# Optimization experiments

Hardware: AMD Instinct MI355X
Metric: run time of the kernel (lower is better)

The kernel has to match this reference:

```python
import jax, jax.numpy as jnp
import numpy as np

N = 50000
E = 640000
F_IN = 96
H1 = 128
H2 = 128
NUM_CLASSES = 256
NGRAM = 3
D1 = 32
L2_EPS = 1e-12


def _prop(xt, src, dst, ew):
    # weighted scatter-add aggregation: out[dst] += ew * xt[src]
    return jax.ops.segment_sum(ew[:, None] * xt[src], dst, num_segments=N)


def _digcn_layer(x, W_mi, W_mo, W_sk, b_mi, b_mo, b_si, b_so, C_in, C_out,
                 ei_in, ew_in, ei_out, ew_out):
    x_sk = x @ W_sk  # skip transform shared by in/out branches
    ic = (_prop(x @ W_mi, ei_in[0], ei_in[1], ew_in) + b_mi
          + _prop(x_sk, ei_in[0], ei_in[1], ew_in) + b_si)
    oc = (_prop(x @ W_mo, ei_out[0], ei_out[1], ew_out) + b_mo
          + _prop(x_sk, ei_out[0], ei_out[1], ew_out) + b_so)
    return C_in * ic + C_out * oc  # C_* are [N,1] vector coefficients


def setup_inputs() -> dict:
    key = jax.random.key(0)
    ks = jax.random.split(key, 32)
    s = 0.05
    d = {
        'x': jax.random.normal(ks[0], (N, F_IN), dtype=jnp.float32),
        'edge_index_in': jax.random.randint(ks[1], (2, E), 0, N, dtype=jnp.int32),
        'edge_weight_in': jax.random.uniform(ks[2], (E,), dtype=jnp.float32),
        'edge_index_out': jax.random.randint(ks[3], (2, E), 0, N, dtype=jnp.int32),
        'edge_weight_out': jax.random.uniform(ks[4], (E,), dtype=jnp.float32),
        'pe_table': jax.random.normal(ks[5], (NGRAM, D1), dtype=jnp.float32) * s,
    }
    dims = [(F_IN, H1), (H1, H1), (H1, H2)]
    ki = 6
    for li, (di, do) in enumerate(dims, start=1):
        d[f'W{li}_main_in'] = jax.random.normal(ks[ki], (di, do), dtype=jnp.float32) * s; ki += 1
        d[f'W{li}_main_out'] = jax.random.normal(ks[ki], (di, do), dtype=jnp.float32) * s; ki += 1
        d[f'W{li}_skip'] = jax.random.normal(ks[ki], (di, do), dtype=jnp.float32) * s; ki += 1
        d[f'b{li}_main_in'] = jax.random.normal(ks[ki], (do,), dtype=jnp.float32) * s; ki += 1
        d[f'b{li}_main_out'] = jax.random.normal(ks[ki], (do,), dtype=jnp.float32) * s; ki += 1
        d[f'b{li}_skip_in'] = jax.random.normal(ks[ki], (do,), dtype=jnp.float32) * s; ki += 1
        d[f'b{li}_skip_out'] = jax.random.normal(ks[ki], (do,), dtype=jnp.float32) * s; ki += 1
        d[f'C{li}_in'] = 1.0 + jax.random.normal(ks[ki], (N, 1), dtype=jnp.float32) * 0.02; ki += 1
        d[f'C{li}_out'] = 1.0 + jax.random.normal(ks[ki], (N, 1), dtype=jnp.float32) * 0.02; ki += 1
    k2 = jax.random.split(ks[ki], 4)
    d['res1_W'] = jax.random.normal(k2[0], (F_IN, H1), dtype=jnp.float32) * s
    d['res1_b'] = jax.random.normal(k2[1], (H1,), dtype=jnp.float32) * s
    d['dec_W'] = jax.random.normal(k2[2], (H2, NUM_CLASSES), dtype=jnp.float32) * s
    d['dec_b'] = jax.random.normal(k2[3], (NUM_CLASSES,), dtype=jnp.float32) * s
    return d


def reference(x, edge_index_in, edge_weight_in, edge_index_out, edge_weight_out, pe_table,
              W1_main_in, W1_main_out, W1_skip, b1_main_in, b1_main_out, b1_skip_in, b1_skip_out, C1_in, C1_out,
              W2_main_in, W2_main_out, W2_skip, b2_main_in, b2_main_out, b2_skip_in, b2_skip_out, C2_in, C2_out,
              W3_main_in, W3_main_out, W3_skip, b3_main_in, b3_main_out, b3_skip_in, b3_skip_out, C3_in, C3_out,
              res1_W, res1_b, dec_W, dec_b):
    # learnable positional encoding: x viewed as [N, ngram, d1] + pe[pos]
    x = (x.reshape(-1, NGRAM, D1) + pe_table[None]).reshape(-1, NGRAM * D1)

    h1 = _digcn_layer(x, W1_main_in, W1_main_out, W1_skip, b1_main_in, b1_main_out,
                      b1_skip_in, b1_skip_out, C1_in, C1_out,
                      edge_index_in, edge_weight_in, edge_index_out, edge_weight_out)
    h1 = jax.nn.relu(h1 + (x @ res1_W + res1_b))  # residual_proj_1 (96 -> 128)

    h2 = _digcn_layer(h1, W2_main_in, W2_main_out, W2_skip, b2_main_in, b2_main_out,
                      b2_skip_in, b2_skip_out, C2_in, C2_out,
                      edge_index_in, edge_weight_in, edge_index_out, edge_weight_out)
    h2 = jax.nn.relu(h2 + h1)  # identity residual (128 == 128)

    h3 = _digcn_layer(h2, W3_main_in, W3_main_out, W3_skip, b3_main_in, b3_main_out,
                      b3_skip_in, b3_skip_out, C3_in, C3_out,
                      edge_index_in, edge_weight_in, edge_index_out, edge_weight_out)
    h3 = h3 + h2  # residual_proj_3 is Identity (hidden1 == hidden2)

    norm = jnp.maximum(jnp.linalg.norm(h3, axis=1, keepdims=True), L2_EPS)
    emb = h3 / norm  # F.normalize, eps=1e-12
    logits = emb @ dec_W + dec_b
    return jax.nn.log_softmax(logits, axis=-1), emb
```

## Files before the change

kernel.cpp:

```cpp
#include <hip/hip_runtime.h>
#include <hip/hip_bf16.h>

typedef unsigned short ushort_t;
typedef __attribute__((ext_vector_type(8))) short bf16x8;
typedef __attribute__((ext_vector_type(4))) float f32x4;

__device__ __forceinline__ float bf2f(ushort_t u) {
    union { unsigned int i; float f; } v; v.i = ((unsigned int)u) << 16; return v.f;
}
__device__ __forceinline__ ushort_t f2bf(float f) {
    unsigned int u = __float_as_uint(f);
    unsigned int r = u + 0x7FFFu + ((u >> 16) & 1u);
    return (ushort_t)(r >> 16);
}
__device__ __forceinline__ float ldf(const void* p, size_t i, int isf) {
    return isf ? ((const float*)p)[i] : bf2f(((const ushort_t*)p)[i]);
}

__global__ void probe_dtype_k(const void* __restrict__ x, int* __restrict__ flag) {
    int t = threadIdx.x;
    const float* xf = (const float*)x;
    int bad = 0;
    for (int i = t; i < 2048; i += 256) {
        unsigned int u = __float_as_uint(xf[i]);
        unsigned int e = (u >> 23) & 0xFFu;
        if (e >= 0xC0u) bad = 1;
    }
    __shared__ int s_bad;
    if (t == 0) s_bad = 0;
    __syncthreads();
    if (bad) atomicOr(&s_bad, 1);
    __syncthreads();
    if (t == 0) flag[0] = s_bad ? 0 : 1;
}

__global__ void count_dst_k(const int* __restrict__ ei, int* __restrict__ cnt, int E) {
    int e = blockIdx.x * 256 + threadIdx.x;
    if (e < E) atomicAdd(&cnt[ei[E + e]], 1);
}

__global__ __launch_bounds__(256) void scan1_k(const int* __restrict__ cntA, const int* __restrict__ cntB,
                                               int* __restrict__ offA, int* __restrict__ offB,
                                               int* __restrict__ sums, int n, int nChunks) {
    int set = blockIdx.y;
    const int* cnt = set ? cntB : cntA;
    int* off = set ? offB : offA;
    __shared__ int s[256];
    int t = threadIdx.x;
    int idx = blockIdx.x * 1024 + t * 4;
    int v[4];
#pragma unroll
    for (int i = 0; i < 4; ++i) v[i] = (idx + i < n) ? cnt[idx + i] : 0;
    int tsum = v[0] + v[1] + v[2] + v[3];
    s[t] = tsum;
    __syncthreads();
    for (int d = 1; d < 256; d <<= 1) {
        int x = (t >= d) ? s[t - d] : 0;
        __syncthreads();
        s[t] += x;
        __syncthreads();
    }
    int run = s[t] - tsum;
    if (t == 255) sums[set * nChunks + blockIdx.x] = s[255];
#pragma unroll
    for (int i = 0; i < 4; ++i) { if (idx + i < n) off[idx + i] = run; run += v[i]; }
}

__global__ __launch_bounds__(256) void scan2_k(int* __restrict__ sums, int nChunks) {
    __shared__ int s[256];
    int t = threadIdx.x;
    for (int set = 0; set < 2; ++set) {
        int v = (t < nChunks) ? sums[set * nChunks + t] : 0;
        s[t] = v;
        __syncthreads();
        for (int d = 1; d < 256; d <<= 1) {
            int x = (t >= d) ? s[t - d] : 0;
            __syncthreads();
            s[t] += x;
            __syncthreads();
        }
        if (t < nChunks) sums[set * nChunks + t] = s[t] - v;
        __syncthreads();
    }
}

__global__ __launch_bounds__(256) void scan3_k(int* __restrict__ offA, int* __restrict__ offB,
                                               const int* __restrict__ sums, int n, int nChunks, int E) {
    int set = blockIdx.y;
    int* off = set ? offB : offA;
    int base = sums[set * nChunks + blockIdx.x];
    int idx = blockIdx.x * 1024 + threadIdx.x * 4;
#pragma unroll
    for (int i = 0; i < 4; ++i) { if (idx + i < n) off[idx + i] += base; }
    if (blockIdx.x == 0 && threadIdx.x == 0) off[n] = E;
}

__global__ void fill_csr_k(const int* __restrict__ ei, const void* __restrict__ ew,
                           const int* __restrict__ off, int* __restrict__ cur,
                           uint2* __restrict__ pairs, int E,
                           const int* __restrict__ flagp) {
    int isf = *flagp;
    int e = blockIdx.x * 256 + threadIdx.x;
    if (e >= E) return;
    int d = ei[E + e];
    int p = off[d] + atomicAdd(&cur[d], 1);
    pairs[p] = make_uint2((unsigned)ei[e], __float_as_uint(ldf(ew, e, isf)));
}

__global__ void prep_bandT_k(ushort_t* __restrict__ Wt, int K, int colOff,
                             const void* __restrict__ A, const void* __restrict__ B, int n,
                             const int* __restrict__ flagp) {
    int isf = *flagp;
    int i = blockIdx.x * 256 + threadIdx.x;
    if (i >= n) return;
    int k = i >> 7, c = i & 127;
    float v = ldf(A, (size_t)k * 128 + c, isf);
    if (B) v += ldf(B, (size_t)k * 128 + c, isf);
    Wt[(size_t)(colOff + c) * K + k] = f2bf(v);
}

__global__ void prep_decT_k(ushort_t* __restrict__ Wdt, const void* __restrict__ W,
                            const int* __restrict__ flagp) {
    int isf = *flagp;
    int i = blockIdx.x * 256 + threadIdx.x;
    int k = i >> 8, c = i & 255;
    Wdt[(size_t)c * 128 + k] = f2bf(ldf(W, (size_t)k * 256 + c, isf));
}

struct BiasJob { const void* a; const void* b; float* dst; int n; };
struct BiasJobs { BiasJob j[8]; };
__global__ void prep_bias_k(BiasJobs jobs, const int* __restrict__ flagp) {
    int isf = *flagp;
    BiasJob jb = jobs.j[blockIdx.x];
    int t = threadIdx.x;
    if (t < jb.n) {
        float v = ldf(jb.a, t, isf);
        if (jb.b) v += ldf(jb.b, t, isf);
        jb.dst[t] = v;
    }
}

template<int K, int DOUT>
__global__ __launch_bounds__(256) void gemm_mfma_k(
    const ushort_t* __restrict__ A, const ushort_t* __restrict__ Wt,
    ushort_t* __restrict__ Y, int M) {
    constexpr int NT = DOUT / 16;
    int tid = threadIdx.x;
    int wave = tid >> 6, lane = tid & 63;
    int q = lane >> 4, l15 = lane & 15;
    int arow = blockIdx.x * 64 + wave * 16 + l15;
    int rowc = arow < M ? arow : M - 1;
    f32x4 acc[NT];
#pragma unroll
    for (int t = 0; t < NT; ++t) acc[t] = (f32x4){0.f, 0.f, 0.f, 0.f};
#pragma unroll
    for (int kc = 0; kc < K; kc += 32) {
        bf16x8 a = *(const bf16x8*)(A + (size_t)rowc * K + kc + q * 8);
#pragma unroll
        for (int t = 0; t < NT; ++t) {
            bf16x8 b = *(const bf16x8*)(Wt + (size_t)(t * 16 + l15) * K + kc + q * 8);
            acc[t] = __builtin_amdgcn_mfma_f32_16x16x32_bf16(a, b, acc[t], 0, 0, 0);
        }
    }
    int outRowBase = blockIdx.x * 64 + wave * 16 + q * 4;
#pragma unroll
    for (int t = 0; t < NT; ++t) {
        int col = t * 16 + l15;
#pragma unroll
        for (int i = 0; i < 4; ++i) {
            int r = outRowBase + i;
            if (r < M) Y[(size_t)r * DOUT + col] = f2bf(acc[t][i]);
        }
    }
}

__global__ __launch_bounds__(256) void gemm_mfma_x_k(
    const void* __restrict__ X, const ushort_t* __restrict__ Wt,
    ushort_t* __restrict__ Y, int M, const void* __restrict__ pe,
    const int* __restrict__ flagp) {
    constexpr int K = 96, DOUT = 384, NT = DOUT / 16;
    __shared__ float pes[96];
    int isf = *flagp;
    int tid = threadIdx.x;
    if (tid < 96) pes[tid] = ldf(pe, tid, isf);
    __syncthreads();
    int wave = tid >> 6, lane = tid & 63;
    int q = lane >> 4, l15 = lane & 15;
    int arow = blockIdx.x * 64 + wave * 16 + l15;
    int rowc = arow < M ? arow : M - 1;
    f32x4 acc[NT];
#pragma unroll
    for (int t = 0; t < NT; ++t) acc[t] = (f32x4){0.f, 0.f, 0.f, 0.f};
#pragma unroll
    for (int kc = 0; kc < K; kc += 32) {
        float va[8];
        size_t base = (size_t)rowc * K + kc + q * 8;
        if (isf) {
            float4 u0 = *(const float4*)((const float*)X + base);
            float4 u1 = *(const float4*)((const float*)X + base + 4);
            va[0] = u0.x; va[1] = u0.y; va[2] = u0.z; va[3] = u0.w;
            va[4] = u1.x; va[5] = u1.y; va[6] = u1.z; va[7] = u1.w;
        } else {
            const ushort_t* xp = (const ushort_t*)X + base;
#pragma unroll
            for (int i = 0; i < 8; ++i) va[i] = bf2f(xp[i]);
        }
        bf16x8 a;
        short* ap = (short*)&a;
#pragma unroll
        for (int i = 0; i < 8; ++i) ap[i] = (short)f2bf(va[i] + pes[kc + q * 8 + i]);
#pragma unroll
        for (int t = 0; t < NT; ++t) {
            bf16x8 b = *(const bf16x8*)(Wt + (size_t)(t * 16 + l15) * K + kc + q * 8);
            acc[t] = __builtin_amdgcn_mfma_f32_16x16x32_bf16(a, b, acc[t], 0, 0, 0);
        }
    }
    int outRowBase = blockIdx.x * 64 + wave * 16 + q * 4;
#pragma unroll
    for (int t = 0; t < NT; ++t) {
        int col = t * 16 + l15;
#pragma unroll
        for (int i = 0; i < 4; ++i) {
            int r = outRowBase + i;
            if (r < M) Y[(size_t)r * DOUT + col] = f2bf(acc[t][i]);
        }
    }
}

__device__ __forceinline__ void gather4(
    const uint2* __restrict__ pairs, const ushort_t* __restrict__ base, int ldY,
    int e0, int e1, float& out0, float& out1) {
    float a0 = 0.f, a1 = 0.f, b0 = 0.f, b1 = 0.f;
    float c0 = 0.f, c1 = 0.f, d0 = 0.f, d1 = 0.f;
    int e = e0;
    for (; e + 4 <= e1; e += 4) {
        uint2 p0 = pairs[e], p1 = pairs[e + 1], p2 = pairs[e + 2], p3 = pairs[e + 3];
        unsigned v0 = *(const unsigned*)(base + (size_t)p0.x * ldY);
        unsigned v1 = *(const unsigned*)(base + (size_t)p1.x * ldY);
        unsigned v2 = *(const unsigned*)(base + (size_t)p2.x * ldY);
        unsigned v3 = *(const unsigned*)(base + (size_t)p3.x * ldY);
        float w0 = __uint_as_float(p0.y), w1 = __uint_as_float(p1.y);
        float w2 = __uint_as_float(p2.y), w3 = __uint_as_float(p3.y);
        a0 += w0 * bf2f((ushort_t)(v0 & 0xffffu)); a1 += w0 * bf2f((ushort_t)(v0 >> 16));
        b0 += w1 * bf2f((ushort_t)(v1 & 0xffffu)); b1 += w1 * bf2f((ushort_t)(v1 >> 16));
        c0 += w2 * bf2f((ushort_t)(v2 & 0xffffu)); c1 += w2 * bf2f((ushort_t)(v2 >> 16));
        d0 += w3 * bf2f((ushort_t)(v3 & 0xffffu)); d1 += w3 * bf2f((ushort_t)(v3 >> 16));
    }
    for (; e < e1; ++e) {
        uint2 p = pairs[e];
        unsigned v = *(const unsigned*)(base + (size_t)p.x * ldY);
        float w = __uint_as_float(p.y);
        a0 += w * bf2f((ushort_t)(v & 0xffffu)); a1 += w * bf2f((ushort_t)(v >> 16));
    }
    out0 = (a0 + b0) + (c0 + d0);
    out1 = (a1 + b1) + (c1 + d1);
}

__global__ __launch_bounds__(256) void prop_combine_k(
    const ushort_t* __restrict__ Y, int ldY,
    const int* __restrict__ offI, const uint2* __restrict__ prI,
    const int* __restrict__ offO, const uint2* __restrict__ prO,
    const void* __restrict__ Cin, const void* __restrict__ Cout,
    const float* __restrict__ bin, const float* __restrict__ bout,
    const ushort_t* __restrict__ res, int ldR, int colR, const float* __restrict__ res_b,
    ushort_t* __restrict__ H, int M, int relu, const int* __restrict__ flagp) {
    int isf = *flagp;
    int node = blockIdx.x * 4 + (threadIdx.x >> 6);
    int lane = threadIdx.x & 63;
    if (node >= M) return;
    float i0, i1, o0, o1;
    gather4(prI, Y + lane * 2,       ldY, offI[node], offI[node + 1], i0, i1);
    gather4(prO, Y + 128 + lane * 2, ldY, offO[node], offO[node + 1], o0, o1);
    int j = lane * 2;
    float ci = ldf(Cin, node, isf), co = ldf(Cout, node, isf);
    float r0 = bf2f(res[(size_t)node * ldR + colR + j]);
    float r1 = bf2f(res[(size_t)node * ldR + colR + j + 1]);
    float v0 = ci * (i0 + bin[j])     + co * (o0 + bout[j])     + r0;
    float v1 = ci * (i1 + bin[j + 1]) + co * (o1 + bout[j + 1]) + r1;
    if (res_b) { v0 += res_b[j]; v1 += res_b[j + 1]; }
    if (relu) { v0 = fmaxf(v0, 0.f); v1 = fmaxf(v1, 0.f); }
    *(unsigned*)(H + (size_t)node * 128 + j) =
        ((unsigned)f2bf(v1) << 16) | (unsigned)f2bf(v0);
}

__global__ __launch_bounds__(256) void decoder_mfma_k(
    const ushort_t* __restrict__ h3, const ushort_t* __restrict__ Wdt,
    const float* __restrict__ biasDec, void* __restrict__ d_out, int M,
    const int* __restrict__ flagp) {
    __shared__ ushort_t embLds[64 * 136];
    __shared__ float sb[256];
    int isf = *flagp;
    int tid = threadIdx.x;
    sb[tid] = biasDec[tid];
    int rowBase = blockIdx.x * 64;
    {
        int r = tid >> 2;
        int c0 = (tid & 3) * 32;
        int grow = rowBase + r;
        uint4 u[4] = {};
        if (grow < M) {
            const uint4* p = (const uint4*)(h3 + (size_t)grow * 128 + c0);
            u[0] = p[0]; u[1] = p[1]; u[2] = p[2]; u[3] = p[3];
        }
        float v[32];
#pragma unroll
        for (int b = 0; b < 4; ++b) {
            unsigned w[4] = {u[b].x, u[b].y, u[b].z, u[b].w};
#pragma unroll
            for (int i = 0; i < 4; ++i) {
                v[b * 8 + 2 * i]     = bf2f((ushort_t)(w[i] & 0xffffu));
                v[b * 8 + 2 * i + 1] = bf2f((ushort_t)(w[i] >> 16));
            }
        }
        float ss = 0.f;
#pragma unroll
        for (int i = 0; i < 32; ++i) ss += v[i] * v[i];
        ss += __shfl_xor(ss, 1, 64);
        ss += __shfl_xor(ss, 2, 64);
        float inv = 1.0f / fmaxf(sqrtf(ss), 1e-12f);
#pragma unroll
        for (int i = 0; i < 32; ++i) v[i] *= inv;
        unsigned* lp = (unsigned*)&embLds[r * 136 + c0];
#pragma unroll
        for (int i = 0; i < 16; ++i)
            lp[i] = ((unsigned)f2bf(v[2 * i + 1]) << 16) | (unsigned)f2bf(v[2 * i]);
        if (grow < M) {
            if (isf) {
                float* op = (float*)d_out + (size_t)M * 256 + (size_t)grow * 128 + c0;
#pragma unroll
                for (int i = 0; i < 32; ++i) op[i] = v[i];
            } else {
                unsigned* op = (unsigned*)((ushort_t*)d_out + (size_t)M * 256 + (size_t)grow * 128 + c0);
#pragma unroll
                for (int i = 0; i < 16; ++i)
                    op[i] = ((unsigned)f2bf(v[2 * i + 1]) << 16) | (unsigned)f2bf(v[2 * i]);
            }
        }
    }
    __syncthreads();
    int wave = tid >> 6, lane = tid & 63, q = lane >> 4, l15 = lane & 15;
    f32x4 acc[16];
#pragma unroll
    for (int t = 0; t < 16; ++t) acc[t] = (f32x4){0.f, 0.f, 0.f, 0.f};
    int ldsRow = wave * 16 + l15;
#pragma unroll
    for (int kc = 0; kc < 128; kc += 32) {
        bf16x8 a = *(const bf16x8*)(&embLds[ldsRow * 136 + kc + q * 8]);
#pragma unroll
        for (int t = 0; t < 16; ++t) {
            bf16x8 b = *(const bf16x8*)(Wdt + (size_t)(t * 16 + l15) * 128 + kc + q * 8);
            acc[t] = __builtin_amdgcn_mfma_f32_16x16x32_bf16(a, b, acc[t], 0, 0, 0);
        }
    }
#pragma unroll
    for (int t = 0; t < 16; ++t) {
        float b = sb[t * 16 + l15];
        acc[t][0] += b; acc[t][1] += b; acc[t][2] += b; acc[t][3] += b;
    }
#pragma unroll
    for (int i = 0; i < 4; ++i) {
        int grow = rowBase + wave * 16 + q * 4 + i;
        float mx = acc[0][i];
#pragma unroll
        for (int t = 1; t < 16; ++t) mx = fmaxf(mx, acc[t][i]);
        mx = fmaxf(mx, __shfl_xor(mx, 1, 64));
        mx = fmaxf(mx, __shfl_xor(mx, 2, 64));
        mx = fmaxf(mx, __shfl_xor(mx, 4, 64));
        mx = fmaxf(mx, __shfl_xor(mx, 8, 64));
        float sm = 0.f;
#pragma unroll
        for (int t = 0; t < 16; ++t) sm += __expf(acc[t][i] - mx);
        sm += __shfl_xor(sm, 1, 64);
        sm += __shfl_xor(sm, 2, 64);
        sm += __shfl_xor(sm, 4, 64);
        sm += __shfl_xor(sm, 8, 64);
        float offv = mx + __logf(sm);
        if (grow < M) {
            if (isf) {
                float* op = (float*)d_out + (size_t)grow * 256 + l15;
#pragma unroll
                for (int t = 0; t < 16; ++t) op[t * 16] = acc[t][i] - offv;
            } else {
                ushort_t* op = (ushort_t*)d_out + (size_t)grow * 256 + l15;
#pragma unroll
                for (int t = 0; t < 16; ++t) op[t * 16] = f2bf(acc[t][i] - offv);
            }
        }
    }
}

extern "C" void kernel_launch(void* const* d_in, const int* in_sizes, int n_in,
                              void* d_out, int out_size, void* d_ws, size_t ws_size,
                              hipStream_t stream) {
    const int N = in_sizes[0] / 96;
    const int E = in_sizes[2];

    const void* x      = d_in[0];
    const int*  ei_in  = (const int*)d_in[1];
    const void* ew_in  = d_in[2];
    const int*  ei_out = (const int*)d_in[3];
    const void* ew_out = d_in[4];
    const void* pe     = d_in[5];

    const void *W_mi[3], *W_mo[3], *W_sk[3], *b_mi[3], *b_mo[3], *b_si[3], *b_so[3], *C_i[3], *C_o[3];
    for (int l = 0; l < 3; ++l) {
        int base = 6 + l * 9;
        W_mi[l] = d_in[base + 0];
        W_mo[l] = d_in[base + 1];
        W_sk[l] = d_in[base + 2];
        b_mi[l] = d_in[base + 3];
        b_mo[l] = d_in[base + 4];
        b_si[l] = d_in[base + 5];
        b_so[l] = d_in[base + 6];
        C_i[l]  = d_in[base + 7];
        C_o[l]  = d_in[base + 8];
    }
    const void* res1_W = d_in[33];
    const void* res1_b = d_in[34];
    const void* dec_W  = d_in[35];
    const void* dec_b  = d_in[36];

    char* ws = (char*)d_ws;
    size_t off = 0;
    auto alloc = [&](size_t bytes) -> void* {
        void* p = ws + off;
        off = (off + bytes + 255) & ~(size_t)255;
        return p;
    };
    const int nChunks = (N + 1023) / 1024;
    int*   flag    = (int*)alloc(4);
    int*   off_in  = (int*)alloc((size_t)(N + 1) * 4);
    int*   cnt_in  = (int*)alloc((size_t)2 * N * 4);
    int*   cur_in  = cnt_in + N;
    uint2* pr_in   = (uint2*)alloc((size_t)E * 8);
    int*   off_out = (int*)alloc((size_t)(N + 1) * 4);
    int*   cnt_out = (int*)alloc((size_t)2 * N * 4);
    int*   cur_out = cnt_out + N;
    uint2* pr_out  = (uint2*)alloc((size_t)E * 8);
    int*   sums    = (int*)alloc((size_t)2 * nChunks * 4);
    ushort_t* Wt1  = (ushort_t*)alloc((size_t)384 * 96 * 2);
    ushort_t* Wt2  = (ushort_t*)alloc((size_t)256 * 128 * 2);
    ushort_t* Wt3  = (ushort_t*)alloc((size_t)256 * 128 * 2);
    ushort_t* Wdt  = (ushort_t*)alloc((size_t)256 * 128 * 2);
    float* biasBlk = (float*)alloc((size_t)1152 * 4);
    float* bin1 = biasBlk, *bout1 = biasBlk + 128, *bin2 = biasBlk + 256, *bout2 = biasBlk + 384;
    float* bin3 = biasBlk + 512, *bout3 = biasBlk + 640, *res1b = biasBlk + 768, *decb = biasBlk + 896;
    ushort_t* Yb  = (ushort_t*)alloc((size_t)N * 384 * 2);
    ushort_t* H1  = (ushort_t*)alloc((size_t)N * 128 * 2);
    ushort_t* H2  = (ushort_t*)alloc((size_t)N * 128 * 2);
    ushort_t* H3  = H1;

    probe_dtype_k<<<1, 256, 0, stream>>>(x, flag);

    hipMemsetAsync(cnt_in, 0, (size_t)2 * N * 4, stream);
    hipMemsetAsync(cnt_out, 0, (size_t)2 * N * 4, stream);
    int egrid = (E + 255) / 256;
    count_dst_k<<<egrid, 256, 0, stream>>>(ei_in, cnt_in, E);
    count_dst_k<<<egrid, 256, 0, stream>>>(ei_out, cnt_out, E);
    {
        dim3 g(nChunks, 2);
        scan1_k<<<g, 256, 0, stream>>>(cnt_in, cnt_out, off_in, off_out, sums, N, nChunks);
        scan2_k<<<1, 256, 0, stream>>>(sums, nChunks);
        scan3_k<<<g, 256, 0, stream>>>(off_in, off_out, sums, N, nChunks, E);
    }
    fill_csr_k<<<egrid, 256, 0, stream>>>(ei_in, ew_in, off_in, cur_in, pr_in, E, flag);
    fill_csr_k<<<egrid, 256, 0, stream>>>(ei_out, ew_out, off_out, cur_out, pr_out, E, flag);

    prep_bandT_k<<<48, 256, 0, stream>>>(Wt1, 96, 0,   W_mi[0], W_sk[0], 128 * 96, flag);
    prep_bandT_k<<<48, 256, 0, stream>>>(Wt1, 96, 128, W_mo[0], W_sk[0], 128 * 96, flag);
    prep_bandT_k<<<48, 256, 0, stream>>>(Wt1, 96, 256, res1_W, (const void*)nullptr, 128 * 96, flag);
    prep_bandT_k<<<64, 256, 0, stream>>>(Wt2, 128, 0,   W_mi[1], W_sk[1], 128 * 128, flag);
    prep_bandT_k<<<64, 256, 0, stream>>>(Wt2, 128, 128, W_mo[1], W_sk[1], 128 * 128, flag);
    prep_bandT_k<<<64, 256, 0, stream>>>(Wt3, 128, 0,   W_mi[2], W_sk[2], 128 * 128, flag);
    prep_bandT_k<<<64, 256, 0, stream>>>(Wt3, 128, 128, W_mo[2], W_sk[2], 128 * 128, flag);
    prep_decT_k<<<128, 256, 0, stream>>>(Wdt, dec_W, flag);
    {
        BiasJobs jb;
        jb.j[0] = {b_mi[0], b_si[0], bin1, 128};
        jb.j[1] = {b_mo[0], b_so[0], bout1, 128};
        jb.j[2] = {b_mi[1], b_si[1], bin2, 128};
        jb.j[3] = {b_mo[1], b_so[1], bout2, 128};
        jb.j[4] = {b_mi[2], b_si[2], bin3, 128};
        jb.j[5] = {b_mo[2], b_so[2], bout3, 128};
        jb.j[6] = {res1_b, nullptr, res1b, 128};
        jb.j[7] = {dec_b, nullptr, decb, 256};
        prep_bias_k<<<8, 256, 0, stream>>>(jb, flag);
    }

    int gBlocks = (N + 63) / 64;
    int pgrid = (N + 3) / 4;

    gemm_mfma_x_k<<<gBlocks, 256, 0, stream>>>(x, Wt1, Yb, N, pe, flag);
    prop_combine_k<<<pgrid, 256, 0, stream>>>(Yb, 384,
        off_in, pr_in, off_out, pr_out,
        C_i[0], C_o[0], bin1, bout1, Yb, 384, 256, res1b, H1, N, 1, flag);
    gemm_mfma_k<128, 256><<<gBlocks, 256, 0, stream>>>(H1, Wt2, Yb, N);
    prop_combine_k<<<pgrid, 256, 0, stream>>>(Yb, 256,
        off_in, pr_in, off_out, pr_out,
        C_i[1], C_o[1], bin2, bout2, H1, 128, 0, (const float*)nullptr, H2, N, 1, flag);
    gemm_mfma_k<128, 256><<<gBlocks, 256, 0, stream>>>(H2, Wt3, Yb, N);
    prop_combine_k<<<pgrid, 256, 0, stream>>>(Yb, 256,
        off_in, pr_in, off_out, pr_out,
        C_i[2], C_o[2], bin3, bout3, H2, 128, 0, (const float*)nullptr, H3, N, 0, flag);
    decoder_mfma_k<<<gBlocks, 256, 0, stream>>>(H3, Wdt, decb, d_out, N, flag);
}
```

Baseline: 667.6 us.

## Unroll edge gather to 8 and vectorize decoder output stores via swapped MFMA

The edge-gather loop is widened from 4 to 8 independent loads in flight, with a 4-wide and scalar tail, to raise memory-level parallelism in the aggregation kernel. In the decoder, the normalized embedding is written out cooperatively from LDS after a barrier, using float4 or uint2 stores instead of per-thread strided scalar writes. The MFMA operands are swapped so each lane holds four consecutive output columns of one row, which allows vectorized log-softmax stores and reduces the cross-lane reductions to two shuffles. The cost is more registers in the gather loop and an extra LDS pass for the embedding write.

```diff
diff --git a/kernel.cpp b/kernel.cpp
--- a/kernel.cpp
+++ b/kernel.cpp
@@ -227,33 +227,50 @@
     }
 }
 
-__device__ __forceinline__ void gather4(
+__device__ __forceinline__ void gather8(
     const uint2* __restrict__ pairs, const ushort_t* __restrict__ base, int ldY,
-    int e0, int e1, float& out0, float& out1) {
-    float a0 = 0.f, a1 = 0.f, b0 = 0.f, b1 = 0.f;
-    float c0 = 0.f, c1 = 0.f, d0 = 0.f, d1 = 0.f;
-    int e = e0;
-    for (; e + 4 <= e1; e += 4) {
-        uint2 p0 = pairs[e], p1 = pairs[e + 1], p2 = pairs[e + 2], p3 = pairs[e + 3];
-        unsigned v0 = *(const unsigned*)(base + (size_t)p0.x * ldY);
-        unsigned v1 = *(const unsigned*)(base + (size_t)p1.x * ldY);
-        unsigned v2 = *(const unsigned*)(base + (size_t)p2.x * ldY);
-        unsigned v3 = *(const unsigned*)(base + (size_t)p3.x * ldY);
-        float w0 = __uint_as_float(p0.y), w1 = __uint_as_float(p1.y);
-        float w2 = __uint_as_float(p2.y), w3 = __uint_as_float(p3.y);
-        a0 += w0 * bf2f((ushort_t)(v0 & 0xffffu)); a1 += w0 * bf2f((ushort_t)(v0 >> 16));
-        b0 += w1 * bf2f((ushort_t)(v1 & 0xffffu)); b1 += w1 * bf2f((ushort_t)(v1 >> 16));
-        c0 += w2 * bf2f((ushort_t)(v2 & 0xffffu)); c1 += w2 * bf2f((ushort_t)(v2 >> 16));
-        d0 += w3 * bf2f((ushort_t)(v3 & 0xffffu)); d1 += w3 * bf2f((ushort_t)(v3 >> 16));
-    }
-    for (; e < e1; ++e) {
+    int eBeg, int eEnd, float& out0, float& out1) {
+    float f0[8] = {0.f, 0.f, 0.f, 0.f, 0.f, 0.f, 0.f, 0.f};
+    float f1[8] = {0.f, 0.f, 0.f, 0.f, 0.f, 0.f, 0.f, 0.f};
+    int e = eBeg;
+    for (; e + 8 <= eEnd; e += 8) {
+        uint2 p[8];
+#pragma unroll
+        for (int u = 0; u < 8; ++u) p[u] = pairs[e + u];
+        unsigned v[8];
+#pragma unroll
+        for (int u = 0; u < 8; ++u) v[u] = *(const unsigned*)(base + (size_t)p[u].x * ldY);
+#pragma unroll
+        for (int u = 0; u < 8; ++u) {
+            float w = __uint_as_float(p[u].y);
+            f0[u] += w * bf2f((ushort_t)(v[u] & 0xffffu));
+            f1[u] += w * bf2f((ushort_t)(v[u] >> 16));
+        }
+    }
+    if (e + 4 <= eEnd) {
+        uint2 p[4];
+#pragma unroll
+        for (int u = 0; u < 4; ++u) p[u] = pairs[e + u];
+        unsigned v[4];
+#pragma unroll
+        for (int u = 0; u < 4; ++u) v[u] = *(const unsigned*)(base + (size_t)p[u].x * ldY);
+#pragma unroll
+        for (int u = 0; u < 4; ++u) {
+            float w = __uint_as_float(p[u].y);
+            f0[u] += w * bf2f((ushort_t)(v[u] & 0xffffu));
+            f1[u] += w * bf2f((ushort_t)(v[u] >> 16));
+        }
+        e += 4;
+    }
+    for (; e < eEnd; ++e) {
         uint2 p = pairs[e];
         unsigned v = *(const unsigned*)(base + (size_t)p.x * ldY);
         float w = __uint_as_float(p.y);
-        a0 += w * bf2f((ushort_t)(v & 0xffffu)); a1 += w * bf2f((ushort_t)(v >> 16));
-    }
-    out0 = (a0 + b0) + (c0 + d0);
-    out1 = (a1 + b1) + (c1 + d1);
+        f0[0] += w * bf2f((ushort_t)(v & 0xffffu));
+        f1[0] += w * bf2f((ushort_t)(v >> 16));
+    }
+    out0 = ((f0[0] + f0[1]) + (f0[2] + f0[3])) + ((f0[4] + f0[5]) + (f0[6] + f0[7]));
+    out1 = ((f1[0] + f1[1]) + (f1[2] + f1[3])) + ((f1[4] + f1[5]) + (f1[6] + f1[7]));
 }
 
 __global__ __launch_bounds__(256) void prop_combine_k(
@@ -269,8 +286,8 @@
     int lane = threadIdx.x & 63;
     if (node >= M) return;
     float i0, i1, o0, o1;
-    gather4(prI, Y + lane * 2,       ldY, offI[node], offI[node + 1], i0, i1);
-    gather4(prO, Y + 128 + lane * 2, ldY, offO[node], offO[node + 1], o0, o1);
+    gather8(prI, Y + lane * 2,       ldY, offI[node], offI[node + 1], i0, i1);
+    gather8(prO, Y + 128 + lane * 2, ldY, offO[node], offO[node + 1], o0, o1);
     int j = lane * 2;
     float ci = ldf(Cin, node, isf), co = ldf(Cout, node, isf);
     float r0 = bf2f(res[(size_t)node * ldR + colR + j]);
@@ -324,20 +341,28 @@
 #pragma unroll
         for (int i = 0; i < 16; ++i)
             lp[i] = ((unsigned)f2bf(v[2 * i + 1]) << 16) | (unsigned)f2bf(v[2 * i]);
-        if (grow < M) {
-            if (isf) {
-                float* op = (float*)d_out + (size_t)M * 256 + (size_t)grow * 128 + c0;
-#pragma unroll
-                for (int i = 0; i < 32; ++i) op[i] = v[i];
-            } else {
-                unsigned* op = (unsigned*)((ushort_t*)d_out + (size_t)M * 256 + (size_t)grow * 128 + c0);
-#pragma unroll
-                for (int i = 0; i < 16; ++i)
-                    op[i] = ((unsigned)f2bf(v[2 * i + 1]) << 16) | (unsigned)f2bf(v[2 * i]);
+    }
+    __syncthreads();
+    {
+        int rowsHere = M - rowBase; if (rowsHere > 64) rowsHere = 64;
+        int total = rowsHere * 128;
+        if (isf) {
+            float* dst = (float*)d_out + (size_t)M * 256 + (size_t)rowBase * 128;
+            for (int idx = tid * 4; idx < total; idx += 1024) {
+                int r = idx >> 7, c = idx & 127;
+                const ushort_t* sp = &embLds[r * 136 + c];
+                float4 o = make_float4(bf2f(sp[0]), bf2f(sp[1]), bf2f(sp[2]), bf2f(sp[3]));
+                *(float4*)(dst + idx) = o;
             }
-        }
-    }
-    __syncthreads();
+        } else {
+            ushort_t* dst = (ushort_t*)d_out + (size_t)M * 256 + (size_t)rowBase * 128;
+            for (int idx = tid * 4; idx < total; idx += 1024) {
+                int r = idx >> 7, c = idx & 127;
+                uint2 o = *(const uint2*)&embLds[r * 136 + c];
+                *(uint2*)(dst + idx) = o;
+            }
+        }
+    }
     int wave = tid >> 6, lane = tid & 63, q = lane >> 4, l15 = lane & 15;
     f32x4 acc[16];
 #pragma unroll
@@ -349,41 +374,48 @@
 #pragma unroll
         for (int t = 0; t < 16; ++t) {
             bf16x8 b = *(const bf16x8*)(Wdt + (size_t)(t * 16 + l15) * 128 + kc + q * 8);
-            acc[t] = __builtin_amdgcn_mfma_f32_16x16x32_bf16(a, b, acc[t], 0, 0, 0);
-        }
-    }
+            acc[t] = __builtin_amdgcn_mfma_f32_16x16x32_bf16(b, a, acc[t], 0, 0, 0);
+        }
+    }
+    int node = rowBase + wave * 16 + l15;
 #pragma unroll
     for (int t = 0; t < 16; ++t) {
-        float b = sb[t * 16 + l15];
-        acc[t][0] += b; acc[t][1] += b; acc[t][2] += b; acc[t][3] += b;
-    }
-#pragma unroll
-    for (int i = 0; i < 4; ++i) {
-        int grow = rowBase + wave * 16 + q * 4 + i;
-        float mx = acc[0][i];
-#pragma unroll
-        for (int t = 1; t < 16; ++t) mx = fmaxf(mx, acc[t][i]);
-        mx = fmaxf(mx, __shfl_xor(mx, 1, 64));
-        mx = fmaxf(mx, __shfl_xor(mx, 2, 64));
-        mx = fmaxf(mx, __shfl_xor(mx, 4, 64));
-        mx = fmaxf(mx, __shfl_xor(mx, 8, 64));
-        float sm = 0.f;
-#pragma unroll
-        for (int t = 0; t < 16; ++t) sm += __expf(acc[t][i] - mx);
-        sm += __shfl_xor(sm, 1, 64);
-        sm += __shfl_xor(sm, 2, 64);
-        sm += __shfl_xor(sm, 4, 64);
-        sm += __shfl_xor(sm, 8, 64);
-        float offv = mx + __logf(sm);
-        if (grow < M) {
-            if (isf) {
-                float* op = (float*)d_out + (size_t)grow * 256 + l15;
-#pragma unroll
-                for (int t = 0; t < 16; ++t) op[t * 16] = acc[t][i] - offv;
-            } else {
-                ushort_t* op = (ushort_t*)d_out + (size_t)grow * 256 + l15;
-#pragma unroll
-                for (int t = 0; t < 16; ++t) op[t * 16] = f2bf(acc[t][i] - offv);
+#pragma unroll
+        for (int i = 0; i < 4; ++i) acc[t][i] += sb[t * 16 + q * 4 + i];
+    }
+    float mx = acc[0][0];
+#pragma unroll
+    for (int t = 0; t < 16; ++t) {
+#pragma unroll
+        for (int i = 0; i < 4; ++i) mx = fmaxf(mx, acc[t][i]);
+    }
+    mx = fmaxf(mx, __shfl_xor(mx, 16, 64));
+    mx = fmaxf(mx, __shfl_xor(mx, 32, 64));
+    float sm = 0.f;
+#pragma unroll
+    for (int t = 0; t < 16; ++t) {
+#pragma unroll
+        for (int i = 0; i < 4; ++i) sm += __expf(acc[t][i] - mx);
+    }
+    sm += __shfl_xor(sm, 16, 64);
+    sm += __shfl_xor(sm, 32, 64);
+    float offv = mx + __logf(sm);
+    if (node < M) {
+        if (isf) {
+            float* op = (float*)d_out + (size_t)node * 256 + q * 4;
+#pragma unroll
+            for (int t = 0; t < 16; ++t) {
+                float4 o = make_float4(acc[t][0] - offv, acc[t][1] - offv,
+                                       acc[t][2] - offv, acc[t][3] - offv);
+                *(float4*)(op + t * 16) = o;
+            }
+        } else {
+            ushort_t* op = (ushort_t*)d_out + (size_t)node * 256 + q * 4;
+#pragma unroll
+            for (int t = 0; t < 16; ++t) {
+                unsigned lo = ((unsigned)f2bf(acc[t][1] - offv) << 16) | (unsigned)f2bf(acc[t][0] - offv);
+                unsigned hi = ((unsigned)f2bf(acc[t][3] - offv) << 16) | (unsigned)f2bf(acc[t][2] - offv);
+                *(uint2*)(op + t * 16) = make_uint2(lo, hi);
             }
         }
     }
```

After: 712.9 us. 1.07x slower.
